# Performance work log

Measured on AMD Instinct MI355X. Metric: run time of the kernel, lower is better.

## Reference

```python
import jax, jax.numpy as jnp
import numpy as np

NEG_INF = -1e38


def _wkv_scan(time_decay, time_first, key, value):
    # key, value: [B, S, D]; time_decay/time_first: [D]
    B, S, D = key.shape
    w = -jnp.exp(time_decay)  # decay applied additively in log-space

    def step(carry, kv):
        num, den, mx = carry
        k, v = kv  # [B, D]
        # output with current token boosted by time_first
        m_out = jnp.maximum(mx, k + time_first)
        e1 = jnp.exp(mx - m_out)
        e2 = jnp.exp(k + time_first - m_out)
        out = (e1 * num + e2 * v) / (e1 * den + e2)
        # state update with decay
        m_new = jnp.maximum(mx + w, k)
        e1 = jnp.exp(mx + w - m_new)
        e2 = jnp.exp(k - m_new)
        return (e1 * num + e2 * v, e1 * den + e2, m_new), out

    init = (jnp.zeros((B, D), jnp.float32),
            jnp.zeros((B, D), jnp.float32),
            jnp.full((B, D), NEG_INF, jnp.float32))
    kv = (jnp.moveaxis(key, 1, 0), jnp.moveaxis(value, 1, 0))  # [S, B, D]
    _, out = jax.lax.scan(step, init, kv)
    return jnp.moveaxis(out, 0, 1)  # [B, S, D]


def setup_inputs() -> dict:
    key = jax.random.key(0)
    ks = jax.random.split(key, 10)
    B, S, H = 4, 2048, 2048
    D = H  # attention_hidden_size
    return {
        "hidden": jax.random.normal(ks[0], (B, S, H), jnp.float32),
        "time_decay": jax.random.normal(ks[1], (D,), jnp.float32),
        "time_first": jax.random.normal(ks[2], (D,), jnp.float32),
        "time_mix_key": jax.random.uniform(ks[3], (1, 1, H), jnp.float32),
        "time_mix_value": jax.random.uniform(ks[4], (1, 1, H), jnp.float32),
        "time_mix_receptance": jax.random.uniform(ks[5], (1, 1, H), jnp.float32),
        "Wk": jax.random.normal(ks[6], (D, H), jnp.float32) / np.sqrt(H),  # torch Linear weight [out, in]
        "Wv": jax.random.normal(ks[7], (D, H), jnp.float32) / np.sqrt(H),
        "Wr": jax.random.normal(ks[8], (D, H), jnp.float32) / np.sqrt(H),
        "Wo": jax.random.normal(ks[9], (H, D), jnp.float32) / np.sqrt(D),
    }


def reference(hidden, time_decay, time_first, time_mix_key, time_mix_value,
              time_mix_receptance, Wk, Wv, Wr, Wo):
    # time_shift: prepend a zero timestep, drop the last (ZeroPad2d((0,0,1,-1)))
    shifted = jnp.pad(hidden, ((0, 0), (1, 0), (0, 0)))[:, :-1]
    xk = hidden * time_mix_key + shifted * (1.0 - time_mix_key)
    xv = hidden * time_mix_value + shifted * (1.0 - time_mix_value)
    xr = hidden * time_mix_receptance + shifted * (1.0 - time_mix_receptance)
    k = jnp.einsum('bsh,dh->bsd', xk, Wk)
    v = jnp.einsum('bsh,dh->bsd', xv, Wv)
    r = jax.nn.sigmoid(jnp.einsum('bsh,dh->bsd', xr, Wr))
    rwkv = _wkv_scan(time_decay, time_first, k, v)
    return jnp.einsum('bsd,hd->bsh', r * rwkv, Wo)
```

## Files before the change

kernel.cpp:

```cpp
#include <hip/hip_runtime.h>


typedef __attribute__((ext_vector_type(8))) short s16x8;
typedef __attribute__((ext_vector_type(4))) float f32x4;

__device__ __forceinline__ unsigned short f2bf(float f) {
  union { float f; unsigned u; } v; v.f = f;
  unsigned r = v.u + 0x7fffu + ((v.u >> 16) & 1u);
  return (unsigned short)(r >> 16);
}
__device__ __forceinline__ float bf2f(unsigned short h) {
  union { unsigned u; float f; } v; v.u = ((unsigned)h) << 16; return v.f;
}
__device__ __forceinline__ void gload_lds16(const void* g, void* l) {
  __builtin_amdgcn_global_load_lds(
      (const __attribute__((address_space(1))) void*)g,
      (__attribute__((address_space(3))) void*)l, 16, 0, 0);
}


__global__ void conv_bf16(const float4* __restrict__ src, ushort4* __restrict__ dst, int n4) {
  int i = blockIdx.x * blockDim.x + threadIdx.x;
  if (i >= n4) return;
  float4 v = src[i];
  ushort4 o;
  o.x = f2bf(v.x); o.y = f2bf(v.y); o.z = f2bf(v.z); o.w = f2bf(v.w);
  dst[i] = o;
}


__global__ void prep_mix3(const float4* __restrict__ hidden,
                          const float4* __restrict__ tmk,
                          const float4* __restrict__ tmv,
                          const float4* __restrict__ tmr,
                          ushort4* __restrict__ xk, ushort4* __restrict__ xv,
                          ushort4* __restrict__ xr,
                          int S, int H4, long long total4) {
  long long i = (long long)blockIdx.x * blockDim.x + threadIdx.x;
  if (i >= total4) return;
  int h4 = (int)(i % H4);
  long long sb = i / H4;
  int s = (int)(sb % S);
  float4 cur = hidden[i];
  float4 prev = make_float4(0.f, 0.f, 0.f, 0.f);
  if (s > 0) prev = hidden[i - H4];
  float4 mk = tmk[h4], mv = tmv[h4], mr = tmr[h4];
  ushort4 ok, ov, orr;
  ok.x = f2bf(cur.x * mk.x + prev.x * (1.f - mk.x));
  ok.y = f2bf(cur.y * mk.y + prev.y * (1.f - mk.y));
  ok.z = f2bf(cur.z * mk.z + prev.z * (1.f - mk.z));
  ok.w = f2bf(cur.w * mk.w + prev.w * (1.f - mk.w));
  ov.x = f2bf(cur.x * mv.x + prev.x * (1.f - mv.x));
  ov.y = f2bf(cur.y * mv.y + prev.y * (1.f - mv.y));
  ov.z = f2bf(cur.z * mv.z + prev.z * (1.f - mv.z));
  ov.w = f2bf(cur.w * mv.w + prev.w * (1.f - mv.w));
  orr.x = f2bf(cur.x * mr.x + prev.x * (1.f - mr.x));
  orr.y = f2bf(cur.y * mr.y + prev.y * (1.f - mr.y));
  orr.z = f2bf(cur.z * mr.z + prev.z * (1.f - mr.z));
  orr.w = f2bf(cur.w * mr.w + prev.w * (1.f - mr.w));
  xk[i] = ok; xv[i] = ov; xr[i] = orr;
}


template <int EPI>
__global__ __launch_bounds__(512, 2) void gemm_bt(
    const unsigned short* __restrict__ A, const unsigned short* __restrict__ B,
    float* __restrict__ Cf, unsigned short* __restrict__ Cb,
    int M, int N, int K) {
  __shared__ unsigned short lds[4 * 16384];

  const int tid = threadIdx.x;
  const int wave = tid >> 6;
  const int lane = tid & 63;

  const int nwg = (int)gridDim.x;
  const int q = nwg >> 3;
  const int wg = (blockIdx.x & 7) * q + (blockIdx.x >> 3);
  const int GM = M >> 8;
  const int bm = (wg % GM) * 256;
  const int bn = (wg / GM) * 256;

  const int wm = (wave >> 2) * 128;
  const int wn = (wave & 3) * 64;
  const int l15 = lane & 15;
  const int lg = lane >> 4;

  f32x4 acc[8][4] = {};

  const int srow = tid >> 2;
  const int sg = ((tid & 3) ^ ((srow >> 1) & 3)) * 8;
  const unsigned short* gA0 = A + (long long)(bm + srow) * K + sg;
  const unsigned short* gA1 = A + (long long)(bm + 128 + srow) * K + sg;
  const unsigned short* gB0 = B + (long long)(bn + srow) * K + sg;
  const unsigned short* gB1 = B + (long long)(bn + 128 + srow) * K + sg;

#define STAGE_A(sl)                                            \
  {                                                            \
    unsigned short* dst = lds + (sl) * 16384 + wave * 512;     \
    gload_lds16(gA0, dst);                                     \
    gload_lds16(gA1, dst + 4096);                              \
    gA0 += 32; gA1 += 32;                                      \
  }
#define STAGE_B(sl)                                            \
  {                                                            \
    unsigned short* dst = lds + (sl) * 16384 + wave * 512;     \
    gload_lds16(gB0, dst + 8192);                              \
    gload_lds16(gB1, dst + 12288);                             \
    gB0 += 32; gB1 += 32;                                      \
  }

  int offA[8], offB[4];
#pragma unroll
  for (int mi = 0; mi < 8; ++mi) {
    int R = wm + mi * 16 + l15;
    offA[mi] = R * 32 + ((lg ^ ((R >> 1) & 3)) * 8);
  }
#pragma unroll
  for (int ni = 0; ni < 4; ++ni) {
    int R = wn + ni * 16 + l15;
    offB[ni] = 8192 + R * 32 + ((lg ^ ((R >> 1) & 3)) * 8);
  }

  const int NT = K >> 5;

  STAGE_A(0); STAGE_B(0);
  STAGE_A(1); STAGE_B(1);
  STAGE_A(2); STAGE_B(2);
  asm volatile("s_waitcnt vmcnt(8)" ::: "memory");
  __builtin_amdgcn_sched_barrier(0);
  __builtin_amdgcn_s_barrier();

  for (int t = 0; t < NT; ++t) {
    const unsigned short* sb = lds + (t & 3) * 16384;
    const bool pf = (t + 3 < NT);

    s16x8 a[4], b[4];
#pragma unroll
    for (int mi = 0; mi < 4; ++mi) a[mi] = *(const s16x8*)(sb + offA[mi]);
#pragma unroll
    for (int ni = 0; ni < 4; ++ni) b[ni] = *(const s16x8*)(sb + offB[ni]);
    if (pf) STAGE_A((t + 3) & 3);
    __builtin_amdgcn_sched_barrier(0);
    __builtin_amdgcn_s_barrier();
    asm volatile("s_waitcnt lgkmcnt(0)" ::: "memory");
    __builtin_amdgcn_sched_barrier(0);
    __builtin_amdgcn_s_setprio(1);
#pragma unroll
    for (int mi = 0; mi < 4; ++mi)
#pragma unroll
      for (int ni = 0; ni < 4; ++ni)
        acc[mi][ni] = __builtin_amdgcn_mfma_f32_16x16x32_bf16(
            a[mi], b[ni], acc[mi][ni], 0, 0, 0);
    __builtin_amdgcn_s_setprio(0);
    __builtin_amdgcn_sched_barrier(0);
    __builtin_amdgcn_s_barrier();

    s16x8 a2[4];
#pragma unroll
    for (int mi = 0; mi < 4; ++mi) a2[mi] = *(const s16x8*)(sb + offA[4 + mi]);
    if (pf) STAGE_B((t + 3) & 3);
    if (pf) {
      asm volatile("s_waitcnt vmcnt(8)" ::: "memory");
    } else if (t + 3 == NT) {
      asm volatile("s_waitcnt vmcnt(4)" ::: "memory");
    } else if (t + 2 == NT) {
      asm volatile("s_waitcnt vmcnt(0)" ::: "memory");
    }
    __builtin_amdgcn_sched_barrier(0);
    __builtin_amdgcn_s_barrier();
    asm volatile("s_waitcnt lgkmcnt(0)" ::: "memory");
    __builtin_amdgcn_sched_barrier(0);
    __builtin_amdgcn_s_setprio(1);
#pragma unroll
    for (int mi = 0; mi < 4; ++mi)
#pragma unroll
      for (int ni = 0; ni < 4; ++ni)
        acc[4 + mi][ni] = __builtin_amdgcn_mfma_f32_16x16x32_bf16(
            a2[mi], b[ni], acc[4 + mi][ni], 0, 0, 0);
    __builtin_amdgcn_s_setprio(0);
    __builtin_amdgcn_sched_barrier(0);
    __builtin_amdgcn_s_barrier();
  }
#undef STAGE_A
#undef STAGE_B

#pragma unroll
  for (int mi = 0; mi < 8; ++mi)
#pragma unroll
    for (int ni = 0; ni < 4; ++ni)
#pragma unroll
      for (int r = 0; r < 4; ++r) {
        int row = bm + wm + mi * 16 + lg * 4 + r;
        int col = bn + wn + ni * 16 + l15;
        float v = acc[mi][ni][r];
        long long idx = (long long)row * N + col;
        if (EPI == 0) {
          Cf[idx] = v;
        } else if (EPI == 1) {
          float s = 1.f / (1.f + __expf(-v));
          Cb[idx] = f2bf(s);
        } else {
          Cb[idx] = f2bf(v);
        }
      }
}


#define NEG_INF_F (-1e38f)

__global__ void scan_phase1(const unsigned short* __restrict__ kb,
                            const unsigned short* __restrict__ vb,
                            const float* __restrict__ td,
                            float* __restrict__ locN, float* __restrict__ locD,
                            float* __restrict__ locM,
                            int S, int D, int C, int L) {
  int t = blockIdx.x * blockDim.x + threadIdx.x;
  int d = t % D;
  int c = (t / D) % C;
  int b = t / (D * C);
  float w = -__expf(td[d]);
  float num = 0.f, den = 0.f, m = NEG_INF_F;
  long long base = ((long long)(b * S + c * L)) * D + d;
  for (int i = 0; i < L; ++i) {
    float kk = bf2f(kb[base]);
    float vv = bf2f(vb[base]);
    base += D;
    float mn = fmaxf(m + w, kk);
    float e1 = __expf(m + w - mn);
    float e2 = __expf(kk - mn);
    num = e1 * num + e2 * vv;
    den = e1 * den + e2;
    m = mn;
  }
  int o = (b * C + c) * D + d;
  locN[o] = num; locD[o] = den; locM[o] = m;
}

__global__ void scan_phase2(const float* __restrict__ td,
                            const float* __restrict__ locN, const float* __restrict__ locD,
                            const float* __restrict__ locM,
                            float* __restrict__ inN, float* __restrict__ inD,
                            float* __restrict__ inM,
                            int Bc, int D, int C, int L) {
  int t = blockIdx.x * blockDim.x + threadIdx.x;
  if (t >= Bc * D) return;
  int d = t % D, b = t / D;
  float w = -__expf(td[d]);
  float Lw = (float)L * w;
  float num = 0.f, den = 0.f, m = NEG_INF_F;
  for (int c = 0; c < C; ++c) {
    int o = (b * C + c) * D + d;
    inN[o] = num; inD[o] = den; inM[o] = m;
    float sm = m + Lw;
    float lm = locM[o];
    float m2 = fmaxf(sm, lm);
    float e1 = __expf(sm - m2);
    float e2 = __expf(lm - m2);
    num = e1 * num + e2 * locN[o];
    den = e1 * den + e2 * locD[o];
    m = m2;
  }
}

__global__ void scan_phase3(const unsigned short* __restrict__ kb,
                            const unsigned short* __restrict__ vb,
                            const unsigned short* __restrict__ rb,
                            const float* __restrict__ td, const float* __restrict__ tfirst,
                            const float* __restrict__ inN, const float* __restrict__ inD,
                            const float* __restrict__ inM,
                            unsigned short* __restrict__ rr,
                            int S, int D, int C, int L) {
  int t = blockIdx.x * blockDim.x + threadIdx.x;
  int d = t % D;
  int c = (t / D) % C;
  int b = t / (D * C);
  float w = -__expf(td[d]);
  float tfd = tfirst[d];
  int o = (b * C + c) * D + d;
  float num = inN[o], den = inD[o], m = inM[o];
  long long base = ((long long)(b * S + c * L)) * D + d;
  for (int i = 0; i < L; ++i) {
    float kk = bf2f(kb[base]);
    float vv = bf2f(vb[base]);
    float rv = bf2f(rb[base]);
    float ktf = kk + tfd;
    float mo = fmaxf(m, ktf);
    float e1 = __expf(m - mo);
    float e2 = __expf(ktf - mo);
    float out = (e1 * num + e2 * vv) / (e1 * den + e2);
    rr[base] = f2bf(out * rv);
    float mn = fmaxf(m + w, kk);
    e1 = __expf(m + w - mn);
    e2 = __expf(kk - mn);
    num = e1 * num + e2 * vv;
    den = e1 * den + e2;
    m = mn;
    base += D;
  }
}


extern "C" void kernel_launch(void* const* d_in, const int* in_sizes, int n_in,
                              void* d_out, int out_size, void* d_ws, size_t ws_size,
                              hipStream_t stream) {
  const float* hidden = (const float*)d_in[0];
  const float* td  = (const float*)d_in[1];
  const float* tfi = (const float*)d_in[2];
  const float* tmk = (const float*)d_in[3];
  const float* tmv = (const float*)d_in[4];
  const float* tmr = (const float*)d_in[5];
  const float* Wk  = (const float*)d_in[6];
  const float* Wv  = (const float*)d_in[7];
  const float* Wr  = (const float*)d_in[8];
  const float* Wo  = (const float*)d_in[9];
  float* out = (float*)d_out;

  const int H = in_sizes[1];
  const int D = H;
  const long long BS = (long long)in_sizes[0] / H;
  const int S = 2048;
  const int B = (int)(BS / S);
  const int C = 32, L = S / C;

  char* ws = (char*)d_ws;
  const size_t MB = 1u << 20;
  unsigned short* W_b = (unsigned short*)(ws + 0 * MB);
  unsigned short* X   = (unsigned short*)(ws + 8 * MB);
  unsigned short* Y   = (unsigned short*)(ws + 40 * MB);
  unsigned short* Z   = (unsigned short*)(ws + 72 * MB);
  float* locN         = (float*)(ws + 104 * MB);
  float* locD         = (float*)(ws + 105 * MB);
  float* locM         = (float*)(ws + 106 * MB);
  float* inN          = (float*)(ws + 107 * MB);
  float* inD          = (float*)(ws + 108 * MB);
  float* inM          = (float*)(ws + 109 * MB);
  unsigned short* kb  = (unsigned short*)out;

  int n4w = H * H / 4;
  int cbk = (n4w + 255) / 256;
  long long total4 = BS * H / 4;
  int pbk = (int)((total4 + 255) / 256);
  int nwg = (int)((BS / 256) * (D / 256));

  prep_mix3<<<pbk, 256, 0, stream>>>((const float4*)hidden,
                                     (const float4*)tmk, (const float4*)tmv, (const float4*)tmr,
                                     (ushort4*)X, (ushort4*)Y, (ushort4*)Z, S, H / 4, total4);

  conv_bf16<<<cbk, 256, 0, stream>>>((const float4*)Wk, (ushort4*)W_b, n4w);
  gemm_bt<2><<<nwg, 512, 0, stream>>>(X, W_b, nullptr, kb, (int)BS, D, H);

  conv_bf16<<<cbk, 256, 0, stream>>>((const float4*)Wv, (ushort4*)W_b, n4w);
  gemm_bt<2><<<nwg, 512, 0, stream>>>(Y, W_b, nullptr, X, (int)BS, D, H);

  conv_bf16<<<cbk, 256, 0, stream>>>((const float4*)Wr, (ushort4*)W_b, n4w);
  gemm_bt<1><<<nwg, 512, 0, stream>>>(Z, W_b, nullptr, Y, (int)BS, D, H);

  int nscan = B * C * D;
  scan_phase1<<<nscan / 256, 256, 0, stream>>>(kb, X, td, locN, locD, locM, S, D, C, L);
  scan_phase2<<<(B * D + 255) / 256, 256, 0, stream>>>(td, locN, locD, locM, inN, inD, inM, B, D, C, L);
  scan_phase3<<<nscan / 256, 256, 0, stream>>>(kb, X, Y, td, tfi, inN, inD, inM, Z, S, D, C, L);

  conv_bf16<<<cbk, 256, 0, stream>>>((const float4*)Wo, (ushort4*)W_b, n4w);
  gemm_bt<0><<<nwg, 512, 0, stream>>>(Z, W_b, out, nullptr, (int)BS, H, D);
}
```

Baseline: 544.2 us.

## Shrink GEMM tile to 128x256 with 3-stage pipeline and vectorize scan kernels

The GEMM workgroup tile is halved in M (128x256) and uses a 3-slot LDS ring with a single combined A/B stage per k-step, allowing more workgroups per CU and a larger grid. The WKV scan kernels now process four channels per thread with ushort4/float4 loads and prefetch of the next timestep into registers. The aim is better occupancy and load balance in the GEMMs and wider memory transactions plus ILP in the scans. The trade-offs are lower per-tile data reuse and fewer scan threads.

```diff
diff --git a/kernel.cpp b/kernel.cpp
--- a/kernel.cpp
+++ b/kernel.cpp
@@ -63,11 +63,11 @@
 
 
 template <int EPI>
-__global__ __launch_bounds__(512, 2) void gemm_bt(
+__global__ __launch_bounds__(512, 4) void gemm_bt(
     const unsigned short* __restrict__ A, const unsigned short* __restrict__ B,
     float* __restrict__ Cf, unsigned short* __restrict__ Cb,
     int M, int N, int K) {
-  __shared__ unsigned short lds[4 * 16384];
+  __shared__ unsigned short lds[3 * 12288];
 
   const int tid = threadIdx.x;
   const int wave = tid >> 6;
@@ -76,93 +76,64 @@
   const int nwg = (int)gridDim.x;
   const int q = nwg >> 3;
   const int wg = (blockIdx.x & 7) * q + (blockIdx.x >> 3);
-  const int GM = M >> 8;
-  const int bm = (wg % GM) * 256;
+  const int GM = M >> 7;
+  const int bm = (wg % GM) * 128;
   const int bn = (wg / GM) * 256;
 
-  const int wm = (wave >> 2) * 128;
+  const int wm = (wave >> 2) * 64;
   const int wn = (wave & 3) * 64;
   const int l15 = lane & 15;
   const int lg = lane >> 4;
 
-  f32x4 acc[8][4] = {};
+  f32x4 acc[4][4] = {};
 
   const int srow = tid >> 2;
   const int sg = ((tid & 3) ^ ((srow >> 1) & 3)) * 8;
-  const unsigned short* gA0 = A + (long long)(bm + srow) * K + sg;
-  const unsigned short* gA1 = A + (long long)(bm + 128 + srow) * K + sg;
+  const unsigned short* gA  = A + (long long)(bm + srow) * K + sg;
   const unsigned short* gB0 = B + (long long)(bn + srow) * K + sg;
   const unsigned short* gB1 = B + (long long)(bn + 128 + srow) * K + sg;
 
-#define STAGE_A(sl)                                            \
+#define STAGE(sl)                                              \
   {                                                            \
-    unsigned short* dst = lds + (sl) * 16384 + wave * 512;     \
-    gload_lds16(gA0, dst);                                     \
-    gload_lds16(gA1, dst + 4096);                              \
-    gA0 += 32; gA1 += 32;                                      \
-  }
-#define STAGE_B(sl)                                            \
-  {                                                            \
-    unsigned short* dst = lds + (sl) * 16384 + wave * 512;     \
-    gload_lds16(gB0, dst + 8192);                              \
-    gload_lds16(gB1, dst + 12288);                             \
-    gB0 += 32; gB1 += 32;                                      \
-  }
-
-  int offA[8], offB[4];
-#pragma unroll
-  for (int mi = 0; mi < 8; ++mi) {
+    unsigned short* d = lds + (sl) * 12288 + wave * 512;       \
+    gload_lds16(gA, d);                                        \
+    gload_lds16(gB0, d + 4096);                                \
+    gload_lds16(gB1, d + 8192);                                \
+    gA += 32; gB0 += 32; gB1 += 32;                            \
+  }
+
+  int offA[4], offB[4];
+#pragma unroll
+  for (int mi = 0; mi < 4; ++mi) {
     int R = wm + mi * 16 + l15;
     offA[mi] = R * 32 + ((lg ^ ((R >> 1) & 3)) * 8);
   }
 #pragma unroll
   for (int ni = 0; ni < 4; ++ni) {
     int R = wn + ni * 16 + l15;
-    offB[ni] = 8192 + R * 32 + ((lg ^ ((R >> 1) & 3)) * 8);
+    offB[ni] = 4096 + R * 32 + ((lg ^ ((R >> 1) & 3)) * 8);
   }
 
   const int NT = K >> 5;
 
-  STAGE_A(0); STAGE_B(0);
-  STAGE_A(1); STAGE_B(1);
-  STAGE_A(2); STAGE_B(2);
-  asm volatile("s_waitcnt vmcnt(8)" ::: "memory");
+  STAGE(0);
+  STAGE(1);
+  asm volatile("s_waitcnt vmcnt(3)" ::: "memory");
   __builtin_amdgcn_sched_barrier(0);
   __builtin_amdgcn_s_barrier();
 
+  int sl0 = 0, sl1 = 1, sl2 = 2;
   for (int t = 0; t < NT; ++t) {
-    const unsigned short* sb = lds + (t & 3) * 16384;
-    const bool pf = (t + 3 < NT);
-
+    const unsigned short* sb = lds + sl0 * 12288;
     s16x8 a[4], b[4];
 #pragma unroll
     for (int mi = 0; mi < 4; ++mi) a[mi] = *(const s16x8*)(sb + offA[mi]);
 #pragma unroll
     for (int ni = 0; ni < 4; ++ni) b[ni] = *(const s16x8*)(sb + offB[ni]);
-    if (pf) STAGE_A((t + 3) & 3);
-    __builtin_amdgcn_sched_barrier(0);
-    __builtin_amdgcn_s_barrier();
-    asm volatile("s_waitcnt lgkmcnt(0)" ::: "memory");
-    __builtin_amdgcn_sched_barrier(0);
-    __builtin_amdgcn_s_setprio(1);
-#pragma unroll
-    for (int mi = 0; mi < 4; ++mi)
-#pragma unroll
-      for (int ni = 0; ni < 4; ++ni)
-        acc[mi][ni] = __builtin_amdgcn_mfma_f32_16x16x32_bf16(
-            a[mi], b[ni], acc[mi][ni], 0, 0, 0);
-    __builtin_amdgcn_s_setprio(0);
-    __builtin_amdgcn_sched_barrier(0);
-    __builtin_amdgcn_s_barrier();
-
-    s16x8 a2[4];
-#pragma unroll
-    for (int mi = 0; mi < 4; ++mi) a2[mi] = *(const s16x8*)(sb + offA[4 + mi]);
-    if (pf) STAGE_B((t + 3) & 3);
-    if (pf) {
-      asm volatile("s_waitcnt vmcnt(8)" ::: "memory");
-    } else if (t + 3 == NT) {
-      asm volatile("s_waitcnt vmcnt(4)" ::: "memory");
+
+    if (t + 2 < NT) {
+      STAGE(sl2);
+      asm volatile("s_waitcnt vmcnt(3)" ::: "memory");
     } else if (t + 2 == NT) {
       asm volatile("s_waitcnt vmcnt(0)" ::: "memory");
     }
@@ -170,22 +141,24 @@
     __builtin_amdgcn_s_barrier();
     asm volatile("s_waitcnt lgkmcnt(0)" ::: "memory");
     __builtin_amdgcn_sched_barrier(0);
+
     __builtin_amdgcn_s_setprio(1);
 #pragma unroll
     for (int mi = 0; mi < 4; ++mi)
 #pragma unroll
       for (int ni = 0; ni < 4; ++ni)
-        acc[4 + mi][ni] = __builtin_amdgcn_mfma_f32_16x16x32_bf16(
-            a2[mi], b[ni], acc[4 + mi][ni], 0, 0, 0);
+        acc[mi][ni] = __builtin_amdgcn_mfma_f32_16x16x32_bf16(
+            a[mi], b[ni], acc[mi][ni], 0, 0, 0);
     __builtin_amdgcn_s_setprio(0);
     __builtin_amdgcn_sched_barrier(0);
     __builtin_amdgcn_s_barrier();
-  }
-#undef STAGE_A
-#undef STAGE_B
-
-#pragma unroll
-  for (int mi = 0; mi < 8; ++mi)
+
+    int tmp = sl0; sl0 = sl1; sl1 = sl2; sl2 = tmp;
+  }
+#undef STAGE
+
+#pragma unroll
+  for (int mi = 0; mi < 4; ++mi)
 #pragma unroll
     for (int ni = 0; ni < 4; ++ni)
 #pragma unroll
@@ -208,94 +181,126 @@
 
 #define NEG_INF_F (-1e38f)
 
-__global__ void scan_phase1(const unsigned short* __restrict__ kb,
-                            const unsigned short* __restrict__ vb,
-                            const float* __restrict__ td,
-                            float* __restrict__ locN, float* __restrict__ locD,
-                            float* __restrict__ locM,
-                            int S, int D, int C, int L) {
+__global__ void scan_phase1(const ushort4* __restrict__ kb,
+                            const ushort4* __restrict__ vb,
+                            const float4* __restrict__ td,
+                            float4* __restrict__ locN, float4* __restrict__ locD,
+                            float4* __restrict__ locM,
+                            int S, int D4, int C, int L) {
   int t = blockIdx.x * blockDim.x + threadIdx.x;
-  int d = t % D;
-  int c = (t / D) % C;
-  int b = t / (D * C);
-  float w = -__expf(td[d]);
-  float num = 0.f, den = 0.f, m = NEG_INF_F;
-  long long base = ((long long)(b * S + c * L)) * D + d;
+  int d = t % D4;
+  int c = (t / D4) % C;
+  int b = t / (D4 * C);
+  float4 tdv = td[d];
+  float w[4] = {-__expf(tdv.x), -__expf(tdv.y), -__expf(tdv.z), -__expf(tdv.w)};
+  float num[4] = {0.f, 0.f, 0.f, 0.f}, den[4] = {0.f, 0.f, 0.f, 0.f};
+  float m[4] = {NEG_INF_F, NEG_INF_F, NEG_INF_F, NEG_INF_F};
+  long long base = (long long)(b * S + c * L) * D4 + d;
+  ushort4 k0 = kb[base], v0 = vb[base];
   for (int i = 0; i < L; ++i) {
-    float kk = bf2f(kb[base]);
-    float vv = bf2f(vb[base]);
-    base += D;
-    float mn = fmaxf(m + w, kk);
-    float e1 = __expf(m + w - mn);
-    float e2 = __expf(kk - mn);
-    num = e1 * num + e2 * vv;
-    den = e1 * den + e2;
-    m = mn;
-  }
-  int o = (b * C + c) * D + d;
-  locN[o] = num; locD[o] = den; locM[o] = m;
-}
-
-__global__ void scan_phase2(const float* __restrict__ td,
-                            const float* __restrict__ locN, const float* __restrict__ locD,
-                            const float* __restrict__ locM,
-                            float* __restrict__ inN, float* __restrict__ inD,
-                            float* __restrict__ inM,
-                            int Bc, int D, int C, int L) {
+    ushort4 k1, v1;
+    if (i + 1 < L) { k1 = kb[base + D4]; v1 = vb[base + D4]; }
+    float kk[4] = {bf2f(k0.x), bf2f(k0.y), bf2f(k0.z), bf2f(k0.w)};
+    float vv[4] = {bf2f(v0.x), bf2f(v0.y), bf2f(v0.z), bf2f(v0.w)};
+#pragma unroll
+    for (int j = 0; j < 4; ++j) {
+      float mn = fmaxf(m[j] + w[j], kk[j]);
+      float e1 = __expf(m[j] + w[j] - mn);
+      float e2 = __expf(kk[j] - mn);
+      num[j] = e1 * num[j] + e2 * vv[j];
+      den[j] = e1 * den[j] + e2;
+      m[j] = mn;
+    }
+    k0 = k1; v0 = v1; base += D4;
+  }
+  int o = (b * C + c) * D4 + d;
+  locN[o] = make_float4(num[0], num[1], num[2], num[3]);
+  locD[o] = make_float4(den[0], den[1], den[2], den[3]);
+  locM[o] = make_float4(m[0], m[1], m[2], m[3]);
+}
+
+__global__ void scan_phase2(const float4* __restrict__ td,
+                            const float4* __restrict__ locN, const float4* __restrict__ locD,
+                            const float4* __restrict__ locM,
+                            float4* __restrict__ inN, float4* __restrict__ inD,
+                            float4* __restrict__ inM,
+                            int Bc, int D4, int C, int L) {
   int t = blockIdx.x * blockDim.x + threadIdx.x;
-  if (t >= Bc * D) return;
-  int d = t % D, b = t / D;
-  float w = -__expf(td[d]);
-  float Lw = (float)L * w;
-  float num = 0.f, den = 0.f, m = NEG_INF_F;
+  if (t >= Bc * D4) return;
+  int d = t % D4, b = t / D4;
+  float4 tdv = td[d];
+  float w[4] = {-__expf(tdv.x), -__expf(tdv.y), -__expf(tdv.z), -__expf(tdv.w)};
+  float num[4] = {0.f, 0.f, 0.f, 0.f}, den[4] = {0.f, 0.f, 0.f, 0.f};
+  float m[4] = {NEG_INF_F, NEG_INF_F, NEG_INF_F, NEG_INF_F};
   for (int c = 0; c < C; ++c) {
-    int o = (b * C + c) * D + d;
-    inN[o] = num; inD[o] = den; inM[o] = m;
-    float sm = m + Lw;
-    float lm = locM[o];
-    float m2 = fmaxf(sm, lm);
-    float e1 = __expf(sm - m2);
-    float e2 = __expf(lm - m2);
-    num = e1 * num + e2 * locN[o];
-    den = e1 * den + e2 * locD[o];
-    m = m2;
-  }
-}
-
-__global__ void scan_phase3(const unsigned short* __restrict__ kb,
-                            const unsigned short* __restrict__ vb,
-                            const unsigned short* __restrict__ rb,
-                            const float* __restrict__ td, const float* __restrict__ tfirst,
-                            const float* __restrict__ inN, const float* __restrict__ inD,
-                            const float* __restrict__ inM,
-                            unsigned short* __restrict__ rr,
-                            int S, int D, int C, int L) {
+    int o = (b * C + c) * D4 + d;
+    inN[o] = make_float4(num[0], num[1], num[2], num[3]);
+    inD[o] = make_float4(den[0], den[1], den[2], den[3]);
+    inM[o] = make_float4(m[0], m[1], m[2], m[3]);
+    float4 lN = locN[o], lD = locD[o], lM = locM[o];
+    float lNa[4] = {lN.x, lN.y, lN.z, lN.w};
+    float lDa[4] = {lD.x, lD.y, lD.z, lD.w};
+    float lMa[4] = {lM.x, lM.y, lM.z, lM.w};
+#pragma unroll
+    for (int j = 0; j < 4; ++j) {
+      float sm = m[j] + (float)L * w[j];
+      float m2 = fmaxf(sm, lMa[j]);
+      float e1 = __expf(sm - m2);
+      float e2 = __expf(lMa[j] - m2);
+      num[j] = e1 * num[j] + e2 * lNa[j];
+      den[j] = e1 * den[j] + e2 * lDa[j];
+      m[j] = m2;
+    }
+  }
+}
+
+__global__ void scan_phase3(const ushort4* __restrict__ kb,
+                            const ushort4* __restrict__ vb,
+                            const ushort4* __restrict__ rb,
+                            const float4* __restrict__ td, const float4* __restrict__ tfirst,
+                            const float4* __restrict__ inN, const float4* __restrict__ inD,
+                            const float4* __restrict__ inM,
+                            ushort4* __restrict__ rr,
+                            int S, int D4, int C, int L) {
   int t = blockIdx.x * blockDim.x + threadIdx.x;
-  int d = t % D;
-  int c = (t / D) % C;
-  int b = t / (D * C);
-  float w = -__expf(td[d]);
-  float tfd = tfirst[d];
-  int o = (b * C + c) * D + d;
-  float num = inN[o], den = inD[o], m = inM[o];
-  long long base = ((long long)(b * S + c * L)) * D + d;
+  int d = t % D4;
+  int c = (t / D4) % C;
+  int b = t / (D4 * C);
+  float4 tdv = td[d], tfv = tfirst[d];
+  float w[4] = {-__expf(tdv.x), -__expf(tdv.y), -__expf(tdv.z), -__expf(tdv.w)};
+  float tf[4] = {tfv.x, tfv.y, tfv.z, tfv.w};
+  int o = (b * C + c) * D4 + d;
+  float4 N0 = inN[o], D0 = inD[o], M0 = inM[o];
+  float num[4] = {N0.x, N0.y, N0.z, N0.w};
+  float den[4] = {D0.x, D0.y, D0.z, D0.w};
+  float m[4] = {M0.x, M0.y, M0.z, M0.w};
+  long long base = (long long)(b * S + c * L) * D4 + d;
+  ushort4 k0 = kb[base], v0 = vb[base], r0 = rb[base];
   for (int i = 0; i < L; ++i) {
-    float kk = bf2f(kb[base]);
-    float vv = bf2f(vb[base]);
-    float rv = bf2f(rb[base]);
-    float ktf = kk + tfd;
-    float mo = fmaxf(m, ktf);
-    float e1 = __expf(m - mo);
-    float e2 = __expf(ktf - mo);
-    float out = (e1 * num + e2 * vv) / (e1 * den + e2);
-    rr[base] = f2bf(out * rv);
-    float mn = fmaxf(m + w, kk);
-    e1 = __expf(m + w - mn);
-    e2 = __expf(kk - mn);
-    num = e1 * num + e2 * vv;
-    den = e1 * den + e2;
-    m = mn;
-    base += D;
+    ushort4 k1, v1, r1;
+    if (i + 1 < L) { k1 = kb[base + D4]; v1 = vb[base + D4]; r1 = rb[base + D4]; }
+    float kk[4] = {bf2f(k0.x), bf2f(k0.y), bf2f(k0.z), bf2f(k0.w)};
+    float vv[4] = {bf2f(v0.x), bf2f(v0.y), bf2f(v0.z), bf2f(v0.w)};
+    float rv[4] = {bf2f(r0.x), bf2f(r0.y), bf2f(r0.z), bf2f(r0.w)};
+    unsigned short ov[4];
+#pragma unroll
+    for (int j = 0; j < 4; ++j) {
+      float ktf = kk[j] + tf[j];
+      float mo = fmaxf(m[j], ktf);
+      float e1 = __expf(m[j] - mo);
+      float e2 = __expf(ktf - mo);
+      float out = (e1 * num[j] + e2 * vv[j]) / (e1 * den[j] + e2);
+      ov[j] = f2bf(out * rv[j]);
+      float mn = fmaxf(m[j] + w[j], kk[j]);
+      e1 = __expf(m[j] + w[j] - mn);
+      e2 = __expf(kk[j] - mn);
+      num[j] = e1 * num[j] + e2 * vv[j];
+      den[j] = e1 * den[j] + e2;
+      m[j] = mn;
+    }
+    ushort4 ow; ow.x = ov[0]; ow.y = ov[1]; ow.z = ov[2]; ow.w = ov[3];
+    rr[base] = ow;
+    k0 = k1; v0 = v1; r0 = r1; base += D4;
   }
 }
 
@@ -321,6 +326,7 @@
   const int S = 2048;
   const int B = (int)(BS / S);
   const int C = 32, L = S / C;
+  const int D4 = D / 4;
 
   char* ws = (char*)d_ws;
   const size_t MB = 1u << 20;
@@ -340,7 +346,7 @@
   int cbk = (n4w + 255) / 256;
   long long total4 = BS * H / 4;
   int pbk = (int)((total4 + 255) / 256);
-  int nwg = (int)((BS / 256) * (D / 256));
+  int nwg = (int)((BS / 128) * (D / 256));
 
   prep_mix3<<<pbk, 256, 0, stream>>>((const float4*)hidden,
                                      (const float4*)tmk, (const float4*)tmv, (const float4*)tmr,
@@ -355,10 +361,18 @@
   conv_bf16<<<cbk, 256, 0, stream>>>((const float4*)Wr, (ushort4*)W_b, n4w);
   gemm_bt<1><<<nwg, 512, 0, stream>>>(Z, W_b, nullptr, Y, (int)BS, D, H);
 
-  int nscan = B * C * D;
-  scan_phase1<<<nscan / 256, 256, 0, stream>>>(kb, X, td, locN, locD, locM, S, D, C, L);
-  scan_phase2<<<(B * D + 255) / 256, 256, 0, stream>>>(td, locN, locD, locM, inN, inD, inM, B, D, C, L);
-  scan_phase3<<<nscan / 256, 256, 0, stream>>>(kb, X, Y, td, tfi, inN, inD, inM, Z, S, D, C, L);
+  int nscan4 = B * C * D4;
+  scan_phase1<<<nscan4 / 256, 256, 0, stream>>>(
+      (const ushort4*)kb, (const ushort4*)X, (const float4*)td,
+      (float4*)locN, (float4*)locD, (float4*)locM, S, D4, C, L);
+  scan_phase2<<<(B * D4 + 255) / 256, 256, 0, stream>>>(
+      (const float4*)td, (const float4*)locN, (const float4*)locD, (const float4*)locM,
+      (float4*)inN, (float4*)inD, (float4*)inM, B, D4, C, L);
+  scan_phase3<<<nscan4 / 256, 256, 0, stream>>>(
+      (const ushort4*)kb, (const ushort4*)X, (const ushort4*)Y,
+      (const float4*)td, (const float4*)tfi,
+      (const float4*)inN, (const float4*)inD, (const float4*)inM,
+      (ushort4*)Z, S, D4, C, L);
 
   conv_bf16<<<cbk, 256, 0, stream>>>((const float4*)Wo, (ushort4*)W_b, n4w);
   gemm_bt<0><<<nwg, 512, 0, stream>>>(Z, W_b, out, nullptr, (int)BS, H, D);
```

Result: slower. 582.3 us (+7.0%).

## Shrink GEMM tile to 128x256 with 3-stage pipeline and batch weight conversion

Applied to the files above, without the earlier changes.

The GEMM block tile drops from 256x256 to 128x256. The LDS pipeline goes from 4 stages with split A/B staging to 3 rotating stages with one combined stage per K step, and launch bounds are raised to allow 4 workgroups per CU. This aims for more workgroups and better occupancy at the cost of less data reuse per tile. The four weight fp32-to-bf16 conversions are merged into one launch that writes all four bf16 weights at once, and workspace buffers are remapped, partly into the output buffer, to make room.

```diff
diff --git a/kernel.cpp b/kernel.cpp
--- a/kernel.cpp
+++ b/kernel.cpp
@@ -19,13 +19,19 @@
 }
 
 
-__global__ void conv_bf16(const float4* __restrict__ src, ushort4* __restrict__ dst, int n4) {
+__global__ void conv_bf16_4(const float4* __restrict__ w0,
+                            const float4* __restrict__ w1,
+                            const float4* __restrict__ w2,
+                            const float4* __restrict__ w3,
+                            ushort4* __restrict__ dst, int n4) {
   int i = blockIdx.x * blockDim.x + threadIdx.x;
   if (i >= n4) return;
+  int w = blockIdx.y;
+  const float4* src = (w == 0) ? w0 : (w == 1) ? w1 : (w == 2) ? w2 : w3;
   float4 v = src[i];
   ushort4 o;
   o.x = f2bf(v.x); o.y = f2bf(v.y); o.z = f2bf(v.z); o.w = f2bf(v.w);
-  dst[i] = o;
+  dst[(long long)w * n4 + i] = o;
 }
 
 
@@ -63,11 +69,11 @@
 
 
 template <int EPI>
-__global__ __launch_bounds__(512, 2) void gemm_bt(
+__global__ __launch_bounds__(512, 4) void gemm_bt(
     const unsigned short* __restrict__ A, const unsigned short* __restrict__ B,
     float* __restrict__ Cf, unsigned short* __restrict__ Cb,
     int M, int N, int K) {
-  __shared__ unsigned short lds[4 * 16384];
+  __shared__ unsigned short lds[3 * 12288];
 
   const int tid = threadIdx.x;
   const int wave = tid >> 6;
@@ -76,93 +82,64 @@
   const int nwg = (int)gridDim.x;
   const int q = nwg >> 3;
   const int wg = (blockIdx.x & 7) * q + (blockIdx.x >> 3);
-  const int GM = M >> 8;
-  const int bm = (wg % GM) * 256;
+  const int GM = M >> 7;
+  const int bm = (wg % GM) * 128;
   const int bn = (wg / GM) * 256;
 
-  const int wm = (wave >> 2) * 128;
+  const int wm = (wave >> 2) * 64;
   const int wn = (wave & 3) * 64;
   const int l15 = lane & 15;
   const int lg = lane >> 4;
 
-  f32x4 acc[8][4] = {};
+  f32x4 acc[4][4] = {};
 
   const int srow = tid >> 2;
   const int sg = ((tid & 3) ^ ((srow >> 1) & 3)) * 8;
-  const unsigned short* gA0 = A + (long long)(bm + srow) * K + sg;
-  const unsigned short* gA1 = A + (long long)(bm + 128 + srow) * K + sg;
+  const unsigned short* gA  = A + (long long)(bm + srow) * K + sg;
   const unsigned short* gB0 = B + (long long)(bn + srow) * K + sg;
   const unsigned short* gB1 = B + (long long)(bn + 128 + srow) * K + sg;
 
-#define STAGE_A(sl)                                            \
+#define STAGE(sl)                                              \
   {                                                            \
-    unsigned short* dst = lds + (sl) * 16384 + wave * 512;     \
-    gload_lds16(gA0, dst);                                     \
-    gload_lds16(gA1, dst + 4096);                              \
-    gA0 += 32; gA1 += 32;                                      \
-  }
-#define STAGE_B(sl)                                            \
-  {                                                            \
-    unsigned short* dst = lds + (sl) * 16384 + wave * 512;     \
-    gload_lds16(gB0, dst + 8192);                              \
-    gload_lds16(gB1, dst + 12288);                             \
-    gB0 += 32; gB1 += 32;                                      \
-  }
-
-  int offA[8], offB[4];
-#pragma unroll
-  for (int mi = 0; mi < 8; ++mi) {
+    unsigned short* d = lds + (sl) * 12288 + wave * 512;       \
+    gload_lds16(gA, d);                                        \
+    gload_lds16(gB0, d + 4096);                                \
+    gload_lds16(gB1, d + 8192);                                \
+    gA += 32; gB0 += 32; gB1 += 32;                            \
+  }
+
+  int offA[4], offB[4];
+#pragma unroll
+  for (int mi = 0; mi < 4; ++mi) {
     int R = wm + mi * 16 + l15;
     offA[mi] = R * 32 + ((lg ^ ((R >> 1) & 3)) * 8);
   }
 #pragma unroll
   for (int ni = 0; ni < 4; ++ni) {
     int R = wn + ni * 16 + l15;
-    offB[ni] = 8192 + R * 32 + ((lg ^ ((R >> 1) & 3)) * 8);
+    offB[ni] = 4096 + R * 32 + ((lg ^ ((R >> 1) & 3)) * 8);
   }
 
   const int NT = K >> 5;
 
-  STAGE_A(0); STAGE_B(0);
-  STAGE_A(1); STAGE_B(1);
-  STAGE_A(2); STAGE_B(2);
-  asm volatile("s_waitcnt vmcnt(8)" ::: "memory");
+  STAGE(0);
+  STAGE(1);
+  asm volatile("s_waitcnt vmcnt(3)" ::: "memory");
   __builtin_amdgcn_sched_barrier(0);
   __builtin_amdgcn_s_barrier();
 
+  int sl0 = 0, sl1 = 1, sl2 = 2;
   for (int t = 0; t < NT; ++t) {
-    const unsigned short* sb = lds + (t & 3) * 16384;
-    const bool pf = (t + 3 < NT);
-
+    const unsigned short* sb = lds + sl0 * 12288;
     s16x8 a[4], b[4];
 #pragma unroll
     for (int mi = 0; mi < 4; ++mi) a[mi] = *(const s16x8*)(sb + offA[mi]);
 #pragma unroll
     for (int ni = 0; ni < 4; ++ni) b[ni] = *(const s16x8*)(sb + offB[ni]);
-    if (pf) STAGE_A((t + 3) & 3);
-    __builtin_amdgcn_sched_barrier(0);
-    __builtin_amdgcn_s_barrier();
-    asm volatile("s_waitcnt lgkmcnt(0)" ::: "memory");
-    __builtin_amdgcn_sched_barrier(0);
-    __builtin_amdgcn_s_setprio(1);
-#pragma unroll
-    for (int mi = 0; mi < 4; ++mi)
-#pragma unroll
-      for (int ni = 0; ni < 4; ++ni)
-        acc[mi][ni] = __builtin_amdgcn_mfma_f32_16x16x32_bf16(
-            a[mi], b[ni], acc[mi][ni], 0, 0, 0);
-    __builtin_amdgcn_s_setprio(0);
-    __builtin_amdgcn_sched_barrier(0);
-    __builtin_amdgcn_s_barrier();
-
-    s16x8 a2[4];
-#pragma unroll
-    for (int mi = 0; mi < 4; ++mi) a2[mi] = *(const s16x8*)(sb + offA[4 + mi]);
-    if (pf) STAGE_B((t + 3) & 3);
-    if (pf) {
-      asm volatile("s_waitcnt vmcnt(8)" ::: "memory");
-    } else if (t + 3 == NT) {
-      asm volatile("s_waitcnt vmcnt(4)" ::: "memory");
+
+    if (t + 2 < NT) {
+      STAGE(sl2);
+      asm volatile("s_waitcnt vmcnt(3)" ::: "memory");
     } else if (t + 2 == NT) {
       asm volatile("s_waitcnt vmcnt(0)" ::: "memory");
     }
@@ -170,22 +147,24 @@
     __builtin_amdgcn_s_barrier();
     asm volatile("s_waitcnt lgkmcnt(0)" ::: "memory");
     __builtin_amdgcn_sched_barrier(0);
+
     __builtin_amdgcn_s_setprio(1);
 #pragma unroll
     for (int mi = 0; mi < 4; ++mi)
 #pragma unroll
       for (int ni = 0; ni < 4; ++ni)
-        acc[4 + mi][ni] = __builtin_amdgcn_mfma_f32_16x16x32_bf16(
-            a2[mi], b[ni], acc[4 + mi][ni], 0, 0, 0);
+        acc[mi][ni] = __builtin_amdgcn_mfma_f32_16x16x32_bf16(
+            a[mi], b[ni], acc[mi][ni], 0, 0, 0);
     __builtin_amdgcn_s_setprio(0);
     __builtin_amdgcn_sched_barrier(0);
     __builtin_amdgcn_s_barrier();
-  }
-#undef STAGE_A
-#undef STAGE_B
-
-#pragma unroll
-  for (int mi = 0; mi < 8; ++mi)
+
+    int tmp = sl0; sl0 = sl1; sl1 = sl2; sl2 = tmp;
+  }
+#undef STAGE
+
+#pragma unroll
+  for (int mi = 0; mi < 4; ++mi)
 #pragma unroll
     for (int ni = 0; ni < 4; ++ni)
 #pragma unroll
@@ -324,42 +303,45 @@
 
   char* ws = (char*)d_ws;
   const size_t MB = 1u << 20;
-  unsigned short* W_b = (unsigned short*)(ws + 0 * MB);
-  unsigned short* X   = (unsigned short*)(ws + 8 * MB);
-  unsigned short* Y   = (unsigned short*)(ws + 40 * MB);
-  unsigned short* Z   = (unsigned short*)(ws + 72 * MB);
-  float* locN         = (float*)(ws + 104 * MB);
-  float* locD         = (float*)(ws + 105 * MB);
-  float* locM         = (float*)(ws + 106 * MB);
-  float* inN          = (float*)(ws + 107 * MB);
-  float* inD          = (float*)(ws + 108 * MB);
-  float* inM          = (float*)(ws + 109 * MB);
-  unsigned short* kb  = (unsigned short*)out;
-
+  unsigned short* Wb  = (unsigned short*)(ws + 0 * MB);
+  unsigned short* Y   = (unsigned short*)(ws + 32 * MB);
+  unsigned short* Z   = (unsigned short*)(ws + 64 * MB);
+  float* locN         = (float*)(ws + 96 * MB);
+  float* locD         = (float*)(ws + 97 * MB);
+  float* locM         = (float*)(ws + 98 * MB);
+  float* inN          = (float*)(ws + 99 * MB);
+  float* inD          = (float*)(ws + 100 * MB);
+  float* inM          = (float*)(ws + 101 * MB);
+
+  unsigned short* kb  = (unsigned short*)d_out;
+  unsigned short* xk  = (unsigned short*)((char*)d_out + 32 * MB);
+  unsigned short* vb  = xk;
+  unsigned short* rb  = Y;
+  unsigned short* rr  = Z;
+
+  const long long HH = (long long)H * H;
   int n4w = H * H / 4;
   int cbk = (n4w + 255) / 256;
   long long total4 = BS * H / 4;
   int pbk = (int)((total4 + 255) / 256);
-  int nwg = (int)((BS / 256) * (D / 256));
+  int nwg = (int)((BS / 128) * (D / 256));
+
+  conv_bf16_4<<<dim3(cbk, 4), 256, 0, stream>>>(
+      (const float4*)Wk, (const float4*)Wv, (const float4*)Wr, (const float4*)Wo,
+      (ushort4*)Wb, n4w);
 
   prep_mix3<<<pbk, 256, 0, stream>>>((const float4*)hidden,
                                      (const float4*)tmk, (const float4*)tmv, (const float4*)tmr,
-                                     (ushort4*)X, (ushort4*)Y, (ushort4*)Z, S, H / 4, total4);
-
-  conv_bf16<<<cbk, 256, 0, stream>>>((const float4*)Wk, (ushort4*)W_b, n4w);
-  gemm_bt<2><<<nwg, 512, 0, stream>>>(X, W_b, nullptr, kb, (int)BS, D, H);
-
-  conv_bf16<<<cbk, 256, 0, stream>>>((const float4*)Wv, (ushort4*)W_b, n4w);
-  gemm_bt<2><<<nwg, 512, 0, stream>>>(Y, W_b, nullptr, X, (int)BS, D, H);
-
-  conv_bf16<<<cbk, 256, 0, stream>>>((const float4*)Wr, (ushort4*)W_b, n4w);
-  gemm_bt<1><<<nwg, 512, 0, stream>>>(Z, W_b, nullptr, Y, (int)BS, D, H);
+                                     (ushort4*)xk, (ushort4*)Y, (ushort4*)Z, S, H / 4, total4);
+
+  gemm_bt<2><<<nwg, 512, 0, stream>>>(xk, Wb + 0 * HH, nullptr, kb, (int)BS, D, H);
+  gemm_bt<2><<<nwg, 512, 0, stream>>>(Y,  Wb + 1 * HH, nullptr, vb, (int)BS, D, H);
+  gemm_bt<1><<<nwg, 512, 0, stream>>>(Z,  Wb + 2 * HH, nullptr, rb, (int)BS, D, H);
 
   int nscan = B * C * D;
-  scan_phase1<<<nscan / 256, 256, 0, stream>>>(kb, X, td, locN, locD, locM, S, D, C, L);
+  scan_phase1<<<nscan / 256, 256, 0, stream>>>(kb, vb, td, locN, locD, locM, S, D, C, L);
   scan_phase2<<<(B * D + 255) / 256, 256, 0, stream>>>(td, locN, locD, locM, inN, inD, inM, B, D, C, L);
-  scan_phase3<<<nscan / 256, 256, 0, stream>>>(kb, X, Y, td, tfi, inN, inD, inM, Z, S, D, C, L);
-
-  conv_bf16<<<cbk, 256, 0, stream>>>((const float4*)Wo, (ushort4*)W_b, n4w);
-  gemm_bt<0><<<nwg, 512, 0, stream>>>(Z, W_b, out, nullptr, (int)BS, H, D);
-}
+  scan_phase3<<<nscan / 256, 256, 0, stream>>>(kb, vb, rb, td, tfi, inN, inD, inM, rr, S, D, C, L);
+
+  gemm_bt<0><<<nwg, 512, 0, stream>>>(rr, Wb + 3 * HH, out, nullptr, (int)BS, H, D);
+}
```

Result: slower. 560.6 us (+3.0%).

## Fuse time-mix into K/V/R GEMM and batch weight conversions into one launch

Applied to the files above, without the earlier changes.

Removes the separate prep_mix3 pass. A new gemm_kvr kernel reads fp32 hidden directly, applies the token-shift mix in registers, converts to bf16 and writes the A tile into LDS. It computes K, V and R in a single launch using a grid y dimension of three. All four weight conversions are merged into one launch, and buffers are rearranged so the three projections can run concurrently. This removes the write and reread of three bf16 activation copies and several launch gaps, but fp32 A loads double the A-side traffic per GEMM and the mix math now sits on the GEMM's critical path, repeated across N tiles.

```diff
diff --git a/kernel.cpp b/kernel.cpp
--- a/kernel.cpp
+++ b/kernel.cpp
@@ -19,46 +19,218 @@
 }
 
 
-__global__ void conv_bf16(const float4* __restrict__ src, ushort4* __restrict__ dst, int n4) {
+__global__ void conv_bf16_4(const float4* __restrict__ w0,
+                            const float4* __restrict__ w1,
+                            const float4* __restrict__ w2,
+                            const float4* __restrict__ w3,
+                            ushort4* __restrict__ dst, int n4) {
   int i = blockIdx.x * blockDim.x + threadIdx.x;
   if (i >= n4) return;
+  int w = blockIdx.y;
+  const float4* src = (w == 0) ? w0 : (w == 1) ? w1 : (w == 2) ? w2 : w3;
   float4 v = src[i];
   ushort4 o;
   o.x = f2bf(v.x); o.y = f2bf(v.y); o.z = f2bf(v.z); o.w = f2bf(v.w);
-  dst[i] = o;
-}
-
-
-__global__ void prep_mix3(const float4* __restrict__ hidden,
-                          const float4* __restrict__ tmk,
-                          const float4* __restrict__ tmv,
-                          const float4* __restrict__ tmr,
-                          ushort4* __restrict__ xk, ushort4* __restrict__ xv,
-                          ushort4* __restrict__ xr,
-                          int S, int H4, long long total4) {
-  long long i = (long long)blockIdx.x * blockDim.x + threadIdx.x;
-  if (i >= total4) return;
-  int h4 = (int)(i % H4);
-  long long sb = i / H4;
-  int s = (int)(sb % S);
-  float4 cur = hidden[i];
-  float4 prev = make_float4(0.f, 0.f, 0.f, 0.f);
-  if (s > 0) prev = hidden[i - H4];
-  float4 mk = tmk[h4], mv = tmv[h4], mr = tmr[h4];
-  ushort4 ok, ov, orr;
-  ok.x = f2bf(cur.x * mk.x + prev.x * (1.f - mk.x));
-  ok.y = f2bf(cur.y * mk.y + prev.y * (1.f - mk.y));
-  ok.z = f2bf(cur.z * mk.z + prev.z * (1.f - mk.z));
-  ok.w = f2bf(cur.w * mk.w + prev.w * (1.f - mk.w));
-  ov.x = f2bf(cur.x * mv.x + prev.x * (1.f - mv.x));
-  ov.y = f2bf(cur.y * mv.y + prev.y * (1.f - mv.y));
-  ov.z = f2bf(cur.z * mv.z + prev.z * (1.f - mv.z));
-  ov.w = f2bf(cur.w * mv.w + prev.w * (1.f - mv.w));
-  orr.x = f2bf(cur.x * mr.x + prev.x * (1.f - mr.x));
-  orr.y = f2bf(cur.y * mr.y + prev.y * (1.f - mr.y));
-  orr.z = f2bf(cur.z * mr.z + prev.z * (1.f - mr.z));
-  orr.w = f2bf(cur.w * mr.w + prev.w * (1.f - mr.w));
-  xk[i] = ok; xv[i] = ov; xr[i] = orr;
+  dst[(long long)w * n4 + i] = o;
+}
+
+
+__global__ __launch_bounds__(512, 2) void gemm_kvr(
+    const float* __restrict__ hidden,
+    const unsigned short* __restrict__ Wb,
+    const float* __restrict__ tmk, const float* __restrict__ tmv,
+    const float* __restrict__ tmr,
+    unsigned short* __restrict__ Ck, unsigned short* __restrict__ Cv,
+    unsigned short* __restrict__ Cr,
+    int M, int N, int K, int S) {
+  __shared__ unsigned short lds[2 * 8192 + 3 * 8192 + 4096];
+  float* ltm = (float*)(lds + 40960);
+
+  const int tid = threadIdx.x;
+  const int wave = tid >> 6;
+  const int lane = tid & 63;
+  const int y = (int)blockIdx.y;
+
+  const unsigned short* B = Wb + (long long)y * N * K;
+  const float* tm = (y == 0) ? tmk : (y == 1) ? tmv : tmr;
+  unsigned short* Cb = (y == 0) ? Ck : (y == 1) ? Cv : Cr;
+
+  const int nwg = (int)gridDim.x;
+  const int q = nwg >> 3;
+  const int wg = (blockIdx.x & 7) * q + (blockIdx.x >> 3);
+  const int GM = M >> 8;
+  const int bm = (wg % GM) * 256;
+  const int bn = (wg / GM) * 256;
+
+  const int wm = (wave >> 2) * 128;
+  const int wn = (wave & 3) * 64;
+  const int l15 = lane & 15;
+  const int lg = lane >> 4;
+
+  f32x4 acc[8][4] = {};
+
+  ((float4*)ltm)[tid] = ((const float4*)tm)[tid];
+  asm volatile("s_waitcnt vmcnt(0) lgkmcnt(0)" ::: "memory");
+  __builtin_amdgcn_sched_barrier(0);
+
+  const int arow = tid >> 1;
+  const int akh = (tid & 1) << 4;
+  const int grow = bm + arow;
+  const int s = grow & (S - 1);
+  const float* hc = hidden + (long long)grow * K + akh;
+  const float* hp = hc - (s > 0 ? K : 0);
+  const float psel = (s > 0) ? 1.f : 0.f;
+  const int ac0 = (tid & 1) * 2;
+  const int aw0 = arow * 32 + (((ac0 + 0) ^ ((arow >> 1) & 3)) << 3);
+  const int aw1 = arow * 32 + (((ac0 + 1) ^ ((arow >> 1) & 3)) << 3);
+
+  float4 hcur[2][4], hprv[2][4];
+
+#define ISSUE_H(pp)                                                   \
+  {                                                                   \
+    _Pragma("unroll") for (int j = 0; j < 4; ++j)                     \
+        hcur[pp][j] = *(const float4*)(hc + 4 * j);                   \
+    _Pragma("unroll") for (int j = 0; j < 4; ++j)                     \
+        hprv[pp][j] = *(const float4*)(hp + 4 * j);                   \
+    hc += 32; hp += 32;                                               \
+  }
+
+#define EXF(v, c) ((c) == 0 ? (v).x : (c) == 1 ? (v).y : (c) == 2 ? (v).z : (v).w)
+
+#define DO_MIX(pp, aslot, tp1)                                        \
+  {                                                                   \
+    unsigned short* ab = lds + (aslot) * 8192;                        \
+    const float* lt = ltm + 32 * (tp1) + akh;                         \
+    float4 tq[4];                                                     \
+    _Pragma("unroll") for (int j = 0; j < 4; ++j)                     \
+        tq[j] = *(const float4*)(lt + 4 * j);                         \
+    unsigned short xs[16];                                            \
+    _Pragma("unroll") for (int j = 0; j < 16; ++j) {                  \
+      float c = EXF(hcur[pp][j >> 2], j & 3);                         \
+      float p = EXF(hprv[pp][j >> 2], j & 3) * psel;                  \
+      float mm = EXF(tq[j >> 2], j & 3);                              \
+      xs[j] = f2bf(c * mm + p * (1.f - mm));                          \
+    }                                                                 \
+    *(s16x8*)(ab + aw0) = *(const s16x8*)&xs[0];                      \
+    *(s16x8*)(ab + aw1) = *(const s16x8*)&xs[8];                      \
+  }
+
+  const int srow = tid >> 2;
+  const int sg = ((tid & 3) ^ ((srow >> 1) & 3)) * 8;
+  const unsigned short* gB0 = B + (long long)(bn + srow) * K + sg;
+  const unsigned short* gB1 = B + (long long)(bn + 128 + srow) * K + sg;
+
+#define STAGE_B(bsl)                                                  \
+  {                                                                   \
+    unsigned short* d = lds + 16384 + (bsl) * 8192 + wave * 512;      \
+    gload_lds16(gB0, d);                                              \
+    gload_lds16(gB1, d + 4096);                                       \
+    gB0 += 32; gB1 += 32;                                             \
+  }
+
+  int offA[8], offB[4];
+#pragma unroll
+  for (int mi = 0; mi < 8; ++mi) {
+    int R = wm + mi * 16 + l15;
+    offA[mi] = R * 32 + ((lg ^ ((R >> 1) & 3)) * 8);
+  }
+#pragma unroll
+  for (int ni = 0; ni < 4; ++ni) {
+    int R = wn + ni * 16 + l15;
+    offB[ni] = R * 32 + ((lg ^ ((R >> 1) & 3)) * 8);
+  }
+
+  const int NT = K >> 5;
+
+  ISSUE_H(0);
+  ISSUE_H(1);
+  STAGE_B(0);
+  STAGE_B(1);
+  asm volatile("s_waitcnt vmcnt(12)" ::: "memory");
+  __builtin_amdgcn_sched_barrier(0);
+  DO_MIX(0, 0, 0);
+  asm volatile("s_waitcnt vmcnt(2)" ::: "memory");
+  __builtin_amdgcn_sched_barrier(0);
+  asm volatile("s_waitcnt lgkmcnt(0)" ::: "memory");
+  __builtin_amdgcn_sched_barrier(0);
+  __builtin_amdgcn_s_barrier();
+
+#define K_ITER(T, PP)                                                         \
+  {                                                                           \
+    const int t_ = (T);                                                       \
+    const unsigned short* aB = lds + ((t_) & 1) * 8192;                       \
+    const unsigned short* bB = lds + 16384 + ((t_) % 3) * 8192;               \
+                                                  \
+    if (t_ + 2 < NT) {                                                        \
+      ISSUE_H(PP);                                                            \
+      asm volatile("s_waitcnt vmcnt(10)" ::: "memory");                       \
+    } else if (t_ + 1 < NT) {                                                 \
+      asm volatile("s_waitcnt vmcnt(2)" ::: "memory");                        \
+    }                                                                         \
+    __builtin_amdgcn_sched_barrier(0);                                        \
+    if (t_ + 1 < NT) DO_MIX(PP ^ 1, (t_ + 1) & 1, t_ + 1);                    \
+    s16x8 a0[4], b0[4];                                                       \
+    _Pragma("unroll") for (int mi = 0; mi < 4; ++mi)                          \
+        a0[mi] = *(const s16x8*)(aB + offA[mi]);                              \
+    _Pragma("unroll") for (int ni = 0; ni < 4; ++ni)                          \
+        b0[ni] = *(const s16x8*)(bB + offB[ni]);                              \
+    __builtin_amdgcn_s_barrier();                                             \
+    asm volatile("s_waitcnt lgkmcnt(0)" ::: "memory");                        \
+    __builtin_amdgcn_sched_barrier(0);                                        \
+    __builtin_amdgcn_s_setprio(1);                                            \
+    _Pragma("unroll") for (int mi = 0; mi < 4; ++mi)                          \
+        _Pragma("unroll") for (int ni = 0; ni < 4; ++ni)                      \
+            acc[mi][ni] = __builtin_amdgcn_mfma_f32_16x16x32_bf16(            \
+                a0[mi], b0[ni], acc[mi][ni], 0, 0, 0);                        \
+    __builtin_amdgcn_s_setprio(0);                                            \
+    __builtin_amdgcn_sched_barrier(0);                                        \
+    __builtin_amdgcn_s_barrier();                                             \
+                                                  \
+    s16x8 a1[4];                                                              \
+    _Pragma("unroll") for (int mi = 0; mi < 4; ++mi)                          \
+        a1[mi] = *(const s16x8*)(aB + offA[4 + mi]);                          \
+    if (t_ + 2 < NT) {                                                        \
+      STAGE_B((t_ + 2) % 3);                                                  \
+      asm volatile("s_waitcnt vmcnt(10)" ::: "memory");                       \
+    } else if (t_ + 1 < NT) {                                                 \
+      asm volatile("s_waitcnt vmcnt(0)" ::: "memory");                        \
+    }                                                                         \
+    __builtin_amdgcn_sched_barrier(0);                                        \
+    __builtin_amdgcn_s_barrier();                                             \
+    asm volatile("s_waitcnt lgkmcnt(0)" ::: "memory");                        \
+    __builtin_amdgcn_sched_barrier(0);                                        \
+    __builtin_amdgcn_s_setprio(1);                                            \
+    _Pragma("unroll") for (int mi = 0; mi < 4; ++mi)                          \
+        _Pragma("unroll") for (int ni = 0; ni < 4; ++ni)                      \
+            acc[4 + mi][ni] = __builtin_amdgcn_mfma_f32_16x16x32_bf16(        \
+                a1[mi], b0[ni], acc[4 + mi][ni], 0, 0, 0);                    \
+    __builtin_amdgcn_s_setprio(0);                                            \
+    __builtin_amdgcn_sched_barrier(0);                                        \
+    __builtin_amdgcn_s_barrier();                                             \
+  }
+
+  for (int t = 0; t < NT; t += 2) {
+    K_ITER(t, 0);
+    K_ITER(t + 1, 1);
+  }
+#undef K_ITER
+#undef STAGE_B
+#undef DO_MIX
+#undef ISSUE_H
+#undef EXF
+
+#pragma unroll
+  for (int mi = 0; mi < 8; ++mi)
+#pragma unroll
+    for (int ni = 0; ni < 4; ++ni)
+#pragma unroll
+      for (int r = 0; r < 4; ++r) {
+        int row = bm + wm + mi * 16 + lg * 4 + r;
+        int col = bn + wn + ni * 16 + l15;
+        float v = acc[mi][ni][r];
+        if (y == 2) v = 1.f / (1.f + __expf(-v));
+        Cb[(long long)row * N + col] = f2bf(v);
+      }
 }
 
 
@@ -324,42 +496,35 @@
 
   char* ws = (char*)d_ws;
   const size_t MB = 1u << 20;
-  unsigned short* W_b = (unsigned short*)(ws + 0 * MB);
-  unsigned short* X   = (unsigned short*)(ws + 8 * MB);
-  unsigned short* Y   = (unsigned short*)(ws + 40 * MB);
-  unsigned short* Z   = (unsigned short*)(ws + 72 * MB);
-  float* locN         = (float*)(ws + 104 * MB);
-  float* locD         = (float*)(ws + 105 * MB);
-  float* locM         = (float*)(ws + 106 * MB);
-  float* inN          = (float*)(ws + 107 * MB);
-  float* inD          = (float*)(ws + 108 * MB);
-  float* inM          = (float*)(ws + 109 * MB);
-  unsigned short* kb  = (unsigned short*)out;
-
+  unsigned short* Wb  = (unsigned short*)(ws + 0 * MB);
+  float* locN         = (float*)(ws + 32 * MB);
+  float* locD         = (float*)(ws + 33 * MB);
+  float* locM         = (float*)(ws + 34 * MB);
+  float* inN          = (float*)(ws + 35 * MB);
+  float* inD          = (float*)(ws + 36 * MB);
+  float* inM          = (float*)(ws + 37 * MB);
+  unsigned short* rb  = (unsigned short*)(ws + 38 * MB);
+  unsigned short* rr  = (unsigned short*)(ws + 70 * MB);
+
+  unsigned short* kb  = (unsigned short*)d_out;
+  unsigned short* vb  = (unsigned short*)((char*)d_out + 32 * MB);
+
+  const long long HH = (long long)H * H;
   int n4w = H * H / 4;
   int cbk = (n4w + 255) / 256;
-  long long total4 = BS * H / 4;
-  int pbk = (int)((total4 + 255) / 256);
   int nwg = (int)((BS / 256) * (D / 256));
 
-  prep_mix3<<<pbk, 256, 0, stream>>>((const float4*)hidden,
-                                     (const float4*)tmk, (const float4*)tmv, (const float4*)tmr,
-                                     (ushort4*)X, (ushort4*)Y, (ushort4*)Z, S, H / 4, total4);
-
-  conv_bf16<<<cbk, 256, 0, stream>>>((const float4*)Wk, (ushort4*)W_b, n4w);
-  gemm_bt<2><<<nwg, 512, 0, stream>>>(X, W_b, nullptr, kb, (int)BS, D, H);
-
-  conv_bf16<<<cbk, 256, 0, stream>>>((const float4*)Wv, (ushort4*)W_b, n4w);
-  gemm_bt<2><<<nwg, 512, 0, stream>>>(Y, W_b, nullptr, X, (int)BS, D, H);
-
-  conv_bf16<<<cbk, 256, 0, stream>>>((const float4*)Wr, (ushort4*)W_b, n4w);
-  gemm_bt<1><<<nwg, 512, 0, stream>>>(Z, W_b, nullptr, Y, (int)BS, D, H);
+  conv_bf16_4<<<dim3(cbk, 4), 256, 0, stream>>>(
+      (const float4*)Wk, (const float4*)Wv, (const float4*)Wr, (const float4*)Wo,
+      (ushort4*)Wb, n4w);
+
+  gemm_kvr<<<dim3(nwg, 3), 512, 0, stream>>>(
+      hidden, Wb, tmk, tmv, tmr, kb, vb, rb, (int)BS, D, H, S);
 
   int nscan = B * C * D;
-  scan_phase1<<<nscan / 256, 256, 0, stream>>>(kb, X, td, locN, locD, locM, S, D, C, L);
+  scan_phase1<<<nscan / 256, 256, 0, stream>>>(kb, vb, td, locN, locD, locM, S, D, C, L);
   scan_phase2<<<(B * D + 255) / 256, 256, 0, stream>>>(td, locN, locD, locM, inN, inD, inM, B, D, C, L);
-  scan_phase3<<<nscan / 256, 256, 0, stream>>>(kb, X, Y, td, tfi, inN, inD, inM, Z, S, D, C, L);
-
-  conv_bf16<<<cbk, 256, 0, stream>>>((const float4*)Wo, (ushort4*)W_b, n4w);
-  gemm_bt<0><<<nwg, 512, 0, stream>>>(Z, W_b, out, nullptr, (int)BS, H, D);
-}
+  scan_phase3<<<nscan / 256, 256, 0, stream>>>(kb, vb, rb, td, tfi, inN, inD, inM, rr, S, D, C, L);
+
+  gemm_bt<0><<<nwg, 512, 0, stream>>>(rr, Wb + 3 * HH, out, nullptr, (int)BS, H, D);
+}
```

New measurement: 733.6 us. +34.8%, slower.
